# Performance work log

Hardware: AMD Instinct MI355X
Metric: run time of the kernel (lower is better)

Reference implementation:

```python
import jax, jax.numpy as jnp
import numpy as np

N, E, LE, C = 20000, 320000, 640000, 128
EPS = 1e-7  # GENConv message eps


def _ln(x, g, b):
    # torch.nn.LayerNorm, eps=1e-5
    m = jnp.mean(x, axis=-1, keepdims=True)
    v = jnp.var(x, axis=-1, keepdims=True)
    return (x - m) * jax.lax.rsqrt(v + 1e-5) * g + b


def _mlp(x, W1, b1, g, b, W2, b2):
    # GENConv MLP, num_layers=2, norm='layer': Linear -> LayerNorm -> ReLU -> Linear
    h = jax.nn.relu(_ln(x @ W1 + b1, g, b))
    return h @ W2 + b2


def _gen_deep(x, src, dst, edge_attr, num_nodes, p):
    # DeepGCNLayer 'res+': norm -> relu -> dropout(eval=identity) -> GENConv -> + x
    h = jax.nn.relu(_ln(x, p['pre_g'], p['pre_b']))
    # GENConv message: relu(x_j [+ edge_attr]) + eps
    msg = h[src]
    if edge_attr is not None:
        msg = msg + edge_attr
    msg = jax.nn.relu(msg) + EPS  # [E, C]
    # softmax aggregation per destination segment, per channel
    logits = msg * p['t']
    mx = jax.ops.segment_max(logits, dst, num_segments=num_nodes)
    alpha = jnp.exp(logits - mx[dst])
    denom = jax.ops.segment_sum(alpha, dst, num_segments=num_nodes)
    aggr = jax.ops.segment_sum(alpha * msg, dst, num_segments=num_nodes)
    aggr = aggr / jnp.where(denom == 0, 1.0, denom)
    out = aggr + h  # GENConv root skip: out + x_r
    out = _mlp(out, p['W1'], p['b1'], p['ln_g'], p['ln_b'], p['W2'], p['b2'])
    return x + out  # res+ residual


def setup_inputs() -> dict:
    key = jax.random.key(0)
    ks = iter(jax.random.split(key, 16))
    s = 0.05
    d = {}
    d['v_x'] = jax.random.normal(next(ks), (N, C), jnp.float32)
    d['e_x'] = jax.random.normal(next(ks), (E, C), jnp.float32)
    d['v_edge_index'] = jax.random.randint(next(ks), (2, E), 0, N)
    d['e_edge_index'] = jax.random.randint(next(ks), (2, LE), 0, E)
    for pfx in ('e_', 'n_'):
        d[pfx + 'pre_g'] = jnp.ones((C,), jnp.float32)
        d[pfx + 'pre_b'] = jnp.zeros((C,), jnp.float32)
        d[pfx + 't'] = jnp.array(1.0, jnp.float32)
        d[pfx + 'W1'] = jax.random.normal(next(ks), (C, 2 * C), jnp.float32) * s
        d[pfx + 'b1'] = jnp.zeros((2 * C,), jnp.float32)
        d[pfx + 'ln_g'] = jnp.ones((2 * C,), jnp.float32)
        d[pfx + 'ln_b'] = jnp.zeros((2 * C,), jnp.float32)
        d[pfx + 'W2'] = jax.random.normal(next(ks), (2 * C, C), jnp.float32) * s
        d[pfx + 'b2'] = jnp.zeros((C,), jnp.float32)
    return d


def reference(v_x, e_x, v_edge_index, e_edge_index,
              e_pre_g, e_pre_b, e_t, e_W1, e_b1, e_ln_g, e_ln_b, e_W2, e_b2,
              n_pre_g, n_pre_b, n_t, n_W1, n_b1, n_ln_g, n_ln_b, n_W2, n_b2):
    ep = dict(pre_g=e_pre_g, pre_b=e_pre_b, t=e_t, W1=e_W1, b1=e_b1,
              ln_g=e_ln_g, ln_b=e_ln_b, W2=e_W2, b2=e_b2)
    npar = dict(pre_g=n_pre_g, pre_b=n_pre_b, t=n_t, W1=n_W1, b1=n_b1,
                ln_g=n_ln_g, ln_b=n_ln_b, W2=n_W2, b2=n_b2)
    # edge layer: GENConv over the line graph (no edge_attr)
    e_out = _gen_deep(e_x, e_edge_index[0], e_edge_index[1], None, E, ep)
    # node layer: GENConv over node graph with updated edge features as edge_attr
    v_out = _gen_deep(v_x, v_edge_index[0], v_edge_index[1], e_out, N, npar)
    return (v_out, e_out)
```

## Files before the change

kernel.cpp:

```cpp
#include <hip/hip_runtime.h>
#include <hip/hip_bf16.h>

#define GEN_EPS 1e-7f

typedef __attribute__((ext_vector_type(8))) short short8;
typedef __attribute__((ext_vector_type(4))) float f32x4;

__global__ void prep_all(
    const float* __restrict__ eW1, const float* __restrict__ eW2,
    const float* __restrict__ nW1, const float* __restrict__ nW2,
    short* __restrict__ eW1P, short* __restrict__ eW2P, short* __restrict__ nW1P,
    short* __restrict__ nW2P,
    const int* __restrict__ e_dst, const int* __restrict__ v_dst,
    int* __restrict__ ce, int* __restrict__ cn, int LE, int En, int nCNT,
    const float* __restrict__ ex, const float* __restrict__ vx,
    const float* __restrict__ eg, const float* __restrict__ eb,
    const float* __restrict__ ng, const float* __restrict__ nb_,
    __hip_bfloat16* __restrict__ he, __hip_bfloat16* __restrict__ hn, int E, int N) {
  int b = blockIdx.x;
  int tid = threadIdx.x;

  if (b < 768) {
    const float* W;
    short* WP;
    int R, Cc, c;
    if (b < 256) {
      W = eW1; WP = eW1P; R = 128; Cc = 256; c = b;
    } else if (b < 384) {
      W = eW2; WP = eW2P; R = 256; Cc = 128; c = b - 256;
    } else if (b < 640) {
      W = nW1; WP = nW1P; R = 128; Cc = 256; c = b - 384;
    } else {
      W = nW2; WP = nW2P; R = 256; Cc = 128; c = b - 640;
    }
    size_t tbase = (size_t)(c >> 4) * (size_t)(16 * R);
    int rsub = c & 15;
    for (int k = tid; k < R; k += blockDim.x) {
      __hip_bfloat16 bv = __float2bfloat16(W[(size_t)k * Cc + c]);
      int kk = k & 31;
      WP[tbase + (size_t)(k >> 5) * 512 + (kk >> 3) * 128 + rsub * 8 + (kk & 7)] =
          *(short*)&bv;
    }
    return;
  }
  b -= 768;

  if (b < nCNT) {
    int i = b * 256 + tid;
    if (i < LE)
      atomicAdd(&ce[e_dst[i]], 1);
    else if (i < LE + En)
      atomicAdd(&cn[v_dst[i - LE]], 1);
    return;
  }
  b -= nCNT;

  int l32 = tid & 31;
  int rr = b * 8 + ((tid & 255) >> 5);
  const float* x;
  const float* g;
  const float* bb;
  __hip_bfloat16* h;
  int r;
  if (rr < E) {
    x = ex; g = eg; bb = eb; h = he; r = rr;
  } else if (rr < E + N) {
    x = vx; g = ng; bb = nb_; h = hn; r = rr - E;
  } else {
    return;
  }
  float4 v = ((const float4*)(x + (size_t)r * 128))[l32];
  float s = v.x + v.y + v.z + v.w;
#pragma unroll
  for (int o = 16; o; o >>= 1) s += __shfl_xor(s, o);
  float m = s * (1.0f / 128.0f);
  float d0 = v.x - m, d1 = v.y - m, d2 = v.z - m, d3 = v.w - m;
  float q = d0 * d0 + d1 * d1 + d2 * d2 + d3 * d3;
#pragma unroll
  for (int o = 16; o; o >>= 1) q += __shfl_xor(q, o);
  float rstd = rsqrtf(q * (1.0f / 128.0f) + 1e-5f);
  float4 gv = ((const float4*)g)[l32];
  float4 bv = ((const float4*)bb)[l32];
  float2 h01, h23;
  h01.x = fmaxf(fmaf(d0 * rstd, gv.x, bv.x), 0.0f);
  h01.y = fmaxf(fmaf(d1 * rstd, gv.y, bv.y), 0.0f);
  h23.x = fmaxf(fmaf(d2 * rstd, gv.z, bv.z), 0.0f);
  h23.y = fmaxf(fmaf(d3 * rstd, gv.w, bv.w), 0.0f);
  __hip_bfloat162 p0 = __float22bfloat162_rn(h01);
  __hip_bfloat162 p1 = __float22bfloat162_rn(h23);
  uint2 u;
  u.x = *(uint*)&p0;
  u.y = *(uint*)&p1;
  ((uint2*)(h + (size_t)r * 128))[l32] = u;
}

__global__ void scan_fused(const int* __restrict__ ce, const int* __restrict__ cn,
                           unsigned long long* __restrict__ part,
                           int* __restrict__ off_e, int* __restrict__ off_n,
                           int* __restrict__ cur_e, int* __restrict__ cur_n,
                           int nbE, int E, int N, int LE, int En) {
  __shared__ int sm[256];
  __shared__ int smPrev;
  int b = blockIdx.x;
  const int* counts;
  int M, nnz, bb;
  int* off;
  int* cursor;
  unsigned long long* pr;
  if (b < nbE) {
    counts = ce; M = E; nnz = LE; bb = b; off = off_e; cursor = cur_e; pr = part;
  } else {
    counts = cn; M = N; nnz = En; bb = b - nbE; off = off_n; cursor = cur_n;
    pr = part + 512;
  }
  int t = threadIdx.x;
  int base = bb * 1024 + t * 4;
  int c[4];
  int s = 0;
#pragma unroll
  for (int i = 0; i < 4; i++) {
    int idx = base + i;
    c[i] = (idx < M) ? counts[idx] : 0;
    s += c[i];
  }
  sm[t] = s;
  __syncthreads();
  for (int o = 1; o < 256; o <<= 1) {
    int v = (t >= o) ? sm[t - o] : 0;
    __syncthreads();
    sm[t] += v;
    __syncthreads();
  }
  int total = sm[255];
  if (t == 0) {
    int prev = 0;
    if (bb == 0) {
      atomicExch(&pr[0], (2ULL << 32) | (unsigned long long)(unsigned)total);
    } else {
      atomicExch(&pr[bb], (1ULL << 32) | (unsigned long long)(unsigned)total);
      int j = bb - 1;
      while (true) {
        unsigned long long v;
        do {
          v = atomicAdd(&pr[j], 0ULL);
        } while ((v >> 32) == 0ULL);
        prev += (int)(v & 0xffffffffULL);
        if ((v >> 32) == 2ULL) break;
        j--;
      }
      atomicExch(&pr[bb], (2ULL << 32) | (unsigned long long)(unsigned)(prev + total));
    }
    smPrev = prev;
  }
  __syncthreads();
  int p = smPrev + sm[t] - s;
#pragma unroll
  for (int i = 0; i < 4; i++) {
    int idx = base + i;
    if (idx < M) {
      off[idx] = p;
      cursor[idx] = p;
      p += c[i];
    }
  }
  if (bb == 0 && t == 0) off[M] = nnz;
}

__global__ void fill_all(const int* __restrict__ e_src, const int* __restrict__ e_dst,
                         const int* __restrict__ v_src, const int* __restrict__ v_dst,
                         int* __restrict__ cur_e, int* __restrict__ cur_n,
                         int* __restrict__ csrs_e, int* __restrict__ csrs_n,
                         int* __restrict__ csre_n, int LE, int En) {
  int i = blockIdx.x * blockDim.x + threadIdx.x;
  if (i < LE) {
    int p = atomicAdd(&cur_e[e_dst[i]], 1);
    csrs_e[p] = e_src[i];
  } else if (i < LE + En) {
    int j = i - LE;
    int p = atomicAdd(&cur_n[v_dst[j]], 1);
    csrs_n[p] = v_src[j];
    csre_n[p] = j;
  }
}

template <bool HAS_EATTR>
__global__ __launch_bounds__(256) void aggregate_kernel(
    const __hip_bfloat16* __restrict__ h, const int* __restrict__ off,
    const int* __restrict__ csr_src, const int* __restrict__ csr_eid,
    const ushort* __restrict__ eattr, const float* __restrict__ tptr,
    uint* __restrict__ yP, int M) {
  int lane = threadIdx.x & 63;
  int r = blockIdx.x * 4 + (threadIdx.x >> 6);
  if (r >= M) return;
  const float t = tptr[0];
  float2 hv = __bfloat1622float2(((const __hip_bfloat162*)(h + (size_t)r * 128))[lane]);
  int e0 = off[r], e1 = off[r + 1];
  float d0 = 0.0f, d1 = 0.0f, a0 = 0.0f, a1 = 0.0f;
  for (int e = e0; e < e1; e += 4) {
    int n = e1 - e;
    float2 mv[4];
#pragma unroll
    for (int u = 0; u < 4; u++) {
      int ee = (u < n) ? e + u : e;
      int s = csr_src[ee];
      mv[u] = __bfloat1622float2(((const __hip_bfloat162*)(h + (size_t)s * 128))[lane]);
    }
    if (HAS_EATTR) {
#pragma unroll
      for (int u = 0; u < 4; u++) {
        int ee = (u < n) ? e + u : e;
        int id = csr_eid[ee];
        uint ea = ((const uint*)(eattr + (size_t)id * 128))[lane];
        float2 ef = __bfloat1622float2(*(__hip_bfloat162*)&ea);
        mv[u].x += ef.x;
        mv[u].y += ef.y;
      }
    }
#pragma unroll
    for (int u = 0; u < 4; u++) {
      float w = (u < n) ? 1.0f : 0.0f;
      float m0 = fmaxf(mv[u].x, 0.0f) + GEN_EPS;
      float m1 = fmaxf(mv[u].y, 0.0f) + GEN_EPS;
      float al0 = __expf(m0 * t) * w, al1 = __expf(m1 * t) * w;
      d0 += al0;
      d1 += al1;
      a0 = fmaf(al0, m0, a0);
      a1 = fmaf(al1, m1, a1);
    }
  }
  float2 yv;
  yv.x = (e1 > e0 ? a0 / d0 : 0.0f) + hv.x;
  yv.y = (e1 > e0 ? a1 / d1 : 0.0f) + hv.y;
  __hip_bfloat162 yb2 = __float22bfloat162_rn(yv);
  yP[(r >> 4) * 1024 + (lane >> 4) * 256 + (r & 15) * 16 + (lane & 15)] = *(uint*)&yb2;
}

template <bool WRITE_BF16>
__global__ __launch_bounds__(512, 2) void mlp_kernel(
    const float* __restrict__ x, const short* yP, const short* __restrict__ W1P,
    const float* __restrict__ b1, const float* __restrict__ lng,
    const float* __restrict__ lnb, const short* __restrict__ W2P,
    const float* __restrict__ b2, float* __restrict__ out, ushort* out16,
    int ntiles, int stride, int M) {
  __shared__ short W1s[128 * 256];
  __shared__ short W2s[256 * 128];
  __shared__ short scr[8][2][16 * 34];

  const int tid = threadIdx.x, lane = tid & 63, wv = tid >> 6;
  const int rA = lane & 15, hi = lane >> 4;
  const int kA = hi * 8, jrow = hi * 4;
  const int foW = lane * 8;
  const int foA = rA * 32 + kA;

  {
    const short8* g1 = (const short8*)W1P;
    short8* l1 = (short8*)W1s;
#pragma unroll
    for (int i = 0; i < 8; i++) l1[i * 512 + tid] = g1[i * 512 + tid];
    const short8* g2 = (const short8*)W2P;
    short8* l2 = (short8*)W2s;
#pragma unroll
    for (int i = 0; i < 8; i++) l2[i * 512 + tid] = g2[i * 512 + tid];
  }

  float b1v[16], lngv[16], lnbv[16], b2v[8];
#pragma unroll
  for (int ct = 0; ct < 16; ct++) {
    int col = ct * 16 + rA;
    b1v[ct] = b1[col];
    lngv[ct] = lng[col];
    lnbv[ct] = lnb[col];
  }
#pragma unroll
  for (int ct = 0; ct < 8; ct++) b2v[ct] = b2[ct * 16 + rA];

  __syncthreads();

  int t = blockIdx.x * 8 + wv;
  short8 yA0, yA1, yA2, yA3;
  if (t < ntiles) {
    const short* yb = yP + (size_t)t * 2048 + foA;
    yA0 = *(const short8*)(yb);
    yA1 = *(const short8*)(yb + 512);
    yA2 = *(const short8*)(yb + 1024);
    yA3 = *(const short8*)(yb + 1536);
  }

  for (; t < ntiles; t += stride) {
    const int row0 = t * 16;

    f32x4 C1[16];
#pragma unroll
    for (int i = 0; i < 16; i++) C1[i] = (f32x4)0.0f;
#pragma unroll
    for (int kc = 0; kc < 4; kc++) {
      short8 a = (kc == 0) ? yA0 : (kc == 1) ? yA1 : (kc == 2) ? yA2 : yA3;
#pragma unroll
      for (int ct = 0; ct < 16; ct++) {
        short8 B = *(const short8*)&W1s[(ct * 4 + kc) * 512 + foW];
        C1[ct] = __builtin_amdgcn_mfma_f32_16x16x32_bf16(a, B, C1[ct], 0, 0, 0);
      }
    }

    {
      int tn = t + stride;
      int tc = (tn < ntiles) ? tn : t;
      const short* yb = yP + (size_t)tc * 2048 + foA;
      yA0 = *(const short8*)(yb);
      yA1 = *(const short8*)(yb + 512);
      yA2 = *(const short8*)(yb + 1024);
      yA3 = *(const short8*)(yb + 1536);
    }

    float xv[32];
#pragma unroll
    for (int ct = 0; ct < 8; ct++)
#pragma unroll
      for (int j = 0; j < 4; j++) {
        int row = row0 + jrow + j;
        int rr = (row < M) ? row : (M - 1);
        xv[ct * 4 + j] = x[(size_t)rr * 128 + ct * 16 + rA];
      }

#pragma unroll
    for (int ct = 0; ct < 16; ct++)
#pragma unroll
      for (int j = 0; j < 4; j++) C1[ct][j] += b1v[ct];

    float mean[4], rstd[4];
#pragma unroll
    for (int j = 0; j < 4; j++) {
      float p = 0.0f, q = 0.0f;
#pragma unroll
      for (int ct = 0; ct < 16; ct++) {
        p += C1[ct][j];
        q = fmaf(C1[ct][j], C1[ct][j], q);
      }
#pragma unroll
      for (int o = 1; o < 16; o <<= 1) {
        p += __shfl_xor(p, o);
        q += __shfl_xor(q, o);
      }
      float m = p * (1.0f / 256.0f);
      mean[j] = m;
      rstd[j] = rsqrtf(q * (1.0f / 256.0f) - m * m + 1e-5f);
    }

    f32x4 C2[8];
#pragma unroll
    for (int i = 0; i < 8; i++) C2[i] = (f32x4)0.0f;
#pragma unroll
    for (int kc = 0; kc < 8; kc++) {
      short* s = &scr[wv][kc & 1][0];
#pragma unroll
      for (int ct2 = 0; ct2 < 2; ct2++) {
        int ctg = kc * 2 + ct2;
#pragma unroll
        for (int j = 0; j < 4; j++) {
          float v =
              fmaxf(fmaf((C1[ctg][j] - mean[j]) * rstd[j], lngv[ctg], lnbv[ctg]), 0.0f);
          __hip_bfloat16 bv = __float2bfloat16(v);
          s[(jrow + j) * 34 + ct2 * 16 + rA] = *(short*)&bv;
        }
      }
      asm volatile("s_waitcnt lgkmcnt(0)" ::: "memory");
      __builtin_amdgcn_sched_barrier(0);
      short8 a = *(const short8*)&s[rA * 34 + kA];
#pragma unroll
      for (int ct = 0; ct < 8; ct++) {
        short8 B = *(const short8*)&W2s[(ct * 8 + kc) * 512 + foW];
        C2[ct] = __builtin_amdgcn_mfma_f32_16x16x32_bf16(a, B, C2[ct], 0, 0, 0);
      }
    }

#pragma unroll
    for (int ct = 0; ct < 8; ct++) {
#pragma unroll
      for (int j = 0; j < 4; j++) {
        int row = row0 + jrow + j;
        if (row < M) {
          size_t idx = (size_t)row * 128 + ct * 16 + rA;
          float o = C2[ct][j] + b2v[ct] + xv[ct * 4 + j];
          out[idx] = o;
          if (WRITE_BF16) {
            __hip_bfloat16 bo = __float2bfloat16(o);
            out16[idx] = *(ushort*)&bo;
          }
        }
      }
    }
  }
}

extern "C" void kernel_launch(void* const* d_in, const int* in_sizes, int n_in,
                              void* d_out, int out_size, void* d_ws, size_t ws_size,
                              hipStream_t stream) {
  const int C = 128;
  const float* v_x = (const float*)d_in[0];
  const float* e_x = (const float*)d_in[1];
  const int* v_ei = (const int*)d_in[2];
  const int* e_ei = (const int*)d_in[3];
  const int N = in_sizes[0] / C;
  const int E = in_sizes[1] / C;
  const int LE = in_sizes[3] / 2;

  const float* ep[9];
  const float* np_[9];
  for (int i = 0; i < 9; i++) ep[i] = (const float*)d_in[4 + i];
  for (int i = 0; i < 9; i++) np_[i] = (const float*)d_in[13 + i];

  float* v_out = (float*)d_out;
  float* e_out = (float*)d_out + (size_t)N * C;

  char* wsp = (char*)d_ws;
  size_t o = 0;
  auto carve = [&](size_t bytes) {
    void* p = wsp + o;
    o += (bytes + 255) & ~(size_t)255;
    return p;
  };
  short* yPe = (short*)carve((size_t)E * C * 2);
  short* yPn = (short*)carve((size_t)N * C * 2);
  int* counts = (int*)carve((size_t)(E + N) * 4);
  unsigned long long* part = (unsigned long long*)carve(1024 * 8);
  int* off_e = (int*)carve(((size_t)E + 1) * 4);
  int* off_n = (int*)carve(((size_t)N + 1) * 4);
  int* cur_e = (int*)carve((size_t)E * 4);
  int* cur_n = (int*)carve((size_t)N * 4);
  int* csrs_e = (int*)carve((size_t)LE * 4);
  int* csrs_n = (int*)carve((size_t)E * 4);
  int* csre_n = (int*)carve((size_t)E * 4);
  short* eW1P = (short*)carve((size_t)256 * 128 * 2);
  short* eW2P = (short*)carve((size_t)128 * 256 * 2);
  short* nW1P = (short*)carve((size_t)256 * 128 * 2);
  short* nW2P = (short*)carve((size_t)128 * 256 * 2);
  (void)ws_size;
  (void)n_in;
  (void)out_size;

  int* counts_e = counts;
  int* counts_n = counts + E;
  __hip_bfloat16* h_e = (__hip_bfloat16*)e_out;
  __hip_bfloat16* h_n = (__hip_bfloat16*)v_out;

  size_t counts_pad = (((size_t)(E + N) * 4) + 255) & ~(size_t)255;
  hipMemsetAsync(counts, 0, counts_pad + 1024 * 8, stream);
  int nCNT = (LE + E + 255) / 256;
  int nLN = (E + N + 7) / 8;
  prep_all<<<768 + nCNT + nLN, 256, 0, stream>>>(
      ep[3], ep[7], np_[3], np_[7], eW1P, eW2P, nW1P, nW2P, e_ei + LE, v_ei + E,
      counts_e, counts_n, LE, E, nCNT, e_x, v_x, ep[0], ep[1], np_[0], np_[1], h_e, h_n,
      E, N);
  int nbE = (E + 1023) / 1024, nbN = (N + 1023) / 1024;
  scan_fused<<<nbE + nbN, 256, 0, stream>>>(counts_e, counts_n, part, off_e, off_n,
                                            cur_e, cur_n, nbE, E, N, LE, E);
  fill_all<<<(LE + E + 255) / 256, 256, 0, stream>>>(e_ei, e_ei + LE, v_ei, v_ei + E,
                                                     cur_e, cur_n, csrs_e, csrs_n, csre_n,
                                                     LE, E);

  aggregate_kernel<false><<<(E + 3) / 4, 256, 0, stream>>>(h_e, off_e, csrs_e, nullptr,
                                                           nullptr, ep[2], (uint*)yPe, E);
  {
    int ntiles = (E + 15) / 16;
    int gblocks = (ntiles + 7) / 8;
    if (gblocks > 256) gblocks = 256;
    int stride = gblocks * 8;
    mlp_kernel<true><<<gblocks, 512, 0, stream>>>(e_x, yPe, eW1P, ep[4], ep[5], ep[6],
                                                  eW2P, ep[8], e_out, (ushort*)yPe,
                                                  ntiles, stride, E);
  }

  aggregate_kernel<true><<<(N + 3) / 4, 256, 0, stream>>>(h_n, off_n, csrs_n, csre_n,
                                                          (const ushort*)yPe, np_[2],
                                                          (uint*)yPn, N);
  {
    int ntiles = (N + 15) / 16;
    int gblocks = (ntiles + 7) / 8;
    if (gblocks > 256) gblocks = 256;
    int stride = gblocks * 8;
    mlp_kernel<false><<<gblocks, 512, 0, stream>>>(v_x, yPn, nW1P, np_[4], np_[5], np_[6],
                                                   nW2P, np_[8], v_out, nullptr, ntiles,
                                                   stride, N);
  }
}
```

Before: 404.4 us.

## Aggregate with half-wave per row, 8-byte gathers, and interleaved src/eid CSR

The aggregation kernel now assigns 32 lanes per destination row instead of 64, with each lane loading 4 bf16 channels (uint2) per neighbor. This doubles the rows per block and widens each gather. The node-graph CSR now stores source and edge id together as an int2, so one load replaces two. The aim is fewer, wider memory transactions and more rows in flight per wave, at the cost of more registers and a more scattered packed-output store pattern.

```diff
diff --git a/kernel.cpp b/kernel.cpp
--- a/kernel.cpp
+++ b/kernel.cpp
@@ -169,8 +169,8 @@
 __global__ void fill_all(const int* __restrict__ e_src, const int* __restrict__ e_dst,
                          const int* __restrict__ v_src, const int* __restrict__ v_dst,
                          int* __restrict__ cur_e, int* __restrict__ cur_n,
-                         int* __restrict__ csrs_e, int* __restrict__ csrs_n,
-                         int* __restrict__ csre_n, int LE, int En) {
+                         int* __restrict__ csrs_e, int2* __restrict__ csrn2,
+                         int LE, int En) {
   int i = blockIdx.x * blockDim.x + threadIdx.x;
   if (i < LE) {
     int p = atomicAdd(&cur_e[e_dst[i]], 1);
@@ -178,61 +178,87 @@
   } else if (i < LE + En) {
     int j = i - LE;
     int p = atomicAdd(&cur_n[v_dst[j]], 1);
-    csrs_n[p] = v_src[j];
-    csre_n[p] = j;
+    int2 st;
+    st.x = v_src[j];
+    st.y = j;
+    csrn2[p] = st;
   }
 }
 
 template <bool HAS_EATTR>
 __global__ __launch_bounds__(256) void aggregate_kernel(
     const __hip_bfloat16* __restrict__ h, const int* __restrict__ off,
-    const int* __restrict__ csr_src, const int* __restrict__ csr_eid,
+    const int* __restrict__ csr_src, const int2* __restrict__ csr2,
     const ushort* __restrict__ eattr, const float* __restrict__ tptr,
     uint* __restrict__ yP, int M) {
-  int lane = threadIdx.x & 63;
-  int r = blockIdx.x * 4 + (threadIdx.x >> 6);
+  int l32 = threadIdx.x & 31;
+  int r = blockIdx.x * 8 + (threadIdx.x >> 5);
   if (r >= M) return;
   const float t = tptr[0];
-  float2 hv = __bfloat1622float2(((const __hip_bfloat162*)(h + (size_t)r * 128))[lane]);
   int e0 = off[r], e1 = off[r + 1];
-  float d0 = 0.0f, d1 = 0.0f, a0 = 0.0f, a1 = 0.0f;
+  float d0 = 0, d1 = 0, d2 = 0, d3 = 0, a0 = 0, a1 = 0, a2 = 0, a3 = 0;
   for (int e = e0; e < e1; e += 4) {
     int n = e1 - e;
-    float2 mv[4];
+    uint2 mraw[4];
+    int ids[4];
 #pragma unroll
     for (int u = 0; u < 4; u++) {
       int ee = (u < n) ? e + u : e;
-      int s = csr_src[ee];
-      mv[u] = __bfloat1622float2(((const __hip_bfloat162*)(h + (size_t)s * 128))[lane]);
-    }
-    if (HAS_EATTR) {
-#pragma unroll
-      for (int u = 0; u < 4; u++) {
-        int ee = (u < n) ? e + u : e;
-        int id = csr_eid[ee];
-        uint ea = ((const uint*)(eattr + (size_t)id * 128))[lane];
-        float2 ef = __bfloat1622float2(*(__hip_bfloat162*)&ea);
-        mv[u].x += ef.x;
-        mv[u].y += ef.y;
-      }
+      int s;
+      if (HAS_EATTR) {
+        int2 se = csr2[ee];
+        s = se.x;
+        ids[u] = se.y;
+      } else {
+        s = csr_src[ee];
+      }
+      mraw[u] = ((const uint2*)(h + (size_t)s * 128))[l32];
     }
 #pragma unroll
     for (int u = 0; u < 4; u++) {
+      float2 lo = __bfloat1622float2(*(__hip_bfloat162*)&mraw[u].x);
+      float2 hi2 = __bfloat1622float2(*(__hip_bfloat162*)&mraw[u].y);
+      if (HAS_EATTR) {
+        uint2 er = ((const uint2*)(eattr + (size_t)ids[u] * 128))[l32];
+        float2 el = __bfloat1622float2(*(__hip_bfloat162*)&er.x);
+        float2 eh = __bfloat1622float2(*(__hip_bfloat162*)&er.y);
+        lo.x += el.x;
+        lo.y += el.y;
+        hi2.x += eh.x;
+        hi2.y += eh.y;
+      }
       float w = (u < n) ? 1.0f : 0.0f;
-      float m0 = fmaxf(mv[u].x, 0.0f) + GEN_EPS;
-      float m1 = fmaxf(mv[u].y, 0.0f) + GEN_EPS;
+      float m0 = fmaxf(lo.x, 0.0f) + GEN_EPS;
+      float m1 = fmaxf(lo.y, 0.0f) + GEN_EPS;
+      float m2 = fmaxf(hi2.x, 0.0f) + GEN_EPS;
+      float m3 = fmaxf(hi2.y, 0.0f) + GEN_EPS;
       float al0 = __expf(m0 * t) * w, al1 = __expf(m1 * t) * w;
+      float al2 = __expf(m2 * t) * w, al3 = __expf(m3 * t) * w;
       d0 += al0;
       d1 += al1;
+      d2 += al2;
+      d3 += al3;
       a0 = fmaf(al0, m0, a0);
       a1 = fmaf(al1, m1, a1);
-    }
-  }
-  float2 yv;
-  yv.x = (e1 > e0 ? a0 / d0 : 0.0f) + hv.x;
-  yv.y = (e1 > e0 ? a1 / d1 : 0.0f) + hv.y;
-  __hip_bfloat162 yb2 = __float22bfloat162_rn(yv);
-  yP[(r >> 4) * 1024 + (lane >> 4) * 256 + (r & 15) * 16 + (lane & 15)] = *(uint*)&yb2;
+      a2 = fmaf(al2, m2, a2);
+      a3 = fmaf(al3, m3, a3);
+    }
+  }
+  uint2 hraw = ((const uint2*)(h + (size_t)r * 128))[l32];
+  float2 hlo = __bfloat1622float2(*(__hip_bfloat162*)&hraw.x);
+  float2 hhi = __bfloat1622float2(*(__hip_bfloat162*)&hraw.y);
+  bool has = e1 > e0;
+  float2 y01, y23;
+  y01.x = (has ? a0 / d0 : 0.0f) + hlo.x;
+  y01.y = (has ? a1 / d1 : 0.0f) + hlo.y;
+  y23.x = (has ? a2 / d2 : 0.0f) + hhi.x;
+  y23.y = (has ? a3 / d3 : 0.0f) + hhi.y;
+  __hip_bfloat162 pb0 = __float22bfloat162_rn(y01);
+  __hip_bfloat162 pb1 = __float22bfloat162_rn(y23);
+  int base = (r >> 4) * 1024 + (r & 15) * 16;
+  int c0 = 2 * l32, c1 = 2 * l32 + 1;
+  yP[base + (c0 >> 4) * 256 + (c0 & 15)] = *(uint*)&pb0;
+  yP[base + (c1 >> 4) * 256 + (c1 & 15)] = *(uint*)&pb1;
 }
 
 template <bool WRITE_BF16>
@@ -428,8 +454,7 @@
   int* cur_e = (int*)carve((size_t)E * 4);
   int* cur_n = (int*)carve((size_t)N * 4);
   int* csrs_e = (int*)carve((size_t)LE * 4);
-  int* csrs_n = (int*)carve((size_t)E * 4);
-  int* csre_n = (int*)carve((size_t)E * 4);
+  int2* csrn2 = (int2*)carve((size_t)E * 8);
   short* eW1P = (short*)carve((size_t)256 * 128 * 2);
   short* eW2P = (short*)carve((size_t)128 * 256 * 2);
   short* nW1P = (short*)carve((size_t)256 * 128 * 2);
@@ -455,11 +480,10 @@
   scan_fused<<<nbE + nbN, 256, 0, stream>>>(counts_e, counts_n, part, off_e, off_n,
                                             cur_e, cur_n, nbE, E, N, LE, E);
   fill_all<<<(LE + E + 255) / 256, 256, 0, stream>>>(e_ei, e_ei + LE, v_ei, v_ei + E,
-                                                     cur_e, cur_n, csrs_e, csrs_n, csre_n,
-                                                     LE, E);
-
-  aggregate_kernel<false><<<(E + 3) / 4, 256, 0, stream>>>(h_e, off_e, csrs_e, nullptr,
-                                                           nullptr, ep[2], (uint*)yPe, E);
+                                                     cur_e, cur_n, csrs_e, csrn2, LE, E);
+
+  aggregate_kernel<false><<<(E + 7) / 8, 256, 0, stream>>>(
+      h_e, off_e, csrs_e, nullptr, nullptr, ep[2], (uint*)yPe, E);
   {
     int ntiles = (E + 15) / 16;
     int gblocks = (ntiles + 7) / 8;
@@ -470,9 +494,8 @@
                                                   ntiles, stride, E);
   }
 
-  aggregate_kernel<true><<<(N + 3) / 4, 256, 0, stream>>>(h_n, off_n, csrs_n, csre_n,
-                                                          (const ushort*)yPe, np_[2],
-                                                          (uint*)yPn, N);
+  aggregate_kernel<true><<<(N + 7) / 8, 256, 0, stream>>>(
+      h_n, off_n, nullptr, csrn2, (const ushort*)yPe, np_[2], (uint*)yPn, N);
   {
     int ntiles = (N + 15) / 16;
     int gblocks = (ntiles + 7) / 8;
```

Result: no change. 401.5 us (-0.7%).
